# Optimization experiments

Measured on AMD Instinct MI355X. Metric: run time of the kernel, lower is better.

Reference implementation:

```python
import jax, jax.numpy as jnp
import numpy as np

LOW_RANK = 8   # q passed to torch.svd_lowrank
NITER = 2      # torch.svd_lowrank default power-iteration count


def setup_inputs() -> dict:
    key = jax.random.key(0)
    k1, k2 = jax.random.split(key)
    x = jax.random.normal(k1, (32, 256, 56, 56), dtype=jnp.float32)
    # Gaussian test matrix used by torch.svd_lowrank's range finder on A^T:
    # R = randn(A.mT.shape[-1]=C, q), shared across the (H*W) batch.
    omega = jax.random.normal(k2, (256, LOW_RANK), dtype=jnp.float32)
    return {"x": x, "omega": omega}


def _qr_q(a):
    # reduced QR, batched over leading dims; inputs are tall (m >= n)
    return jnp.linalg.qr(a, mode="reduced")[0]


def reference(x, omega):
    B, C, H, W = x.shape
    # [B,C,H,W] -> [H,W,C,B] -> (H*W, C, B): H*W small matrices A of shape (C, B)
    A = jnp.transpose(x, (2, 3, 1, 0)).reshape(H * W, C, B)

    # torch.svd_lowrank with n=B > q takes the transposed branch:
    #   Q = get_approximate_basis(A^T, q, niter=2)   (Q: (B, q), orthonormal cols)
    #   U S V^T == (A @ Q) @ Q^T  -> reconstruction is A Q Q^T
    Y = jnp.einsum("mcb,cq->mbq", A, omega)      # A^T @ Omega : (M, B, q)
    Q = _qr_q(Y)
    for _ in range(NITER):
        Z = jnp.einsum("mcb,mbq->mcq", A, Q)     # A @ Q       : (M, C, q)
        Qc = _qr_q(Z)
        Y = jnp.einsum("mcb,mcq->mbq", A, Qc)    # A^T @ Qc    : (M, B, q)
        Q = _qr_q(Y)

    P = jnp.einsum("mcb,mbq->mcq", A, Q)         # A @ Q       : (M, C, q)
    y = jnp.einsum("mcq,mbq->mcb", P, Q)         # A Q Q^T     : (M, C, B)

    y = y.reshape(H, W, C, B)
    return jnp.transpose(y, (3, 2, 0, 1))        # back to [B, C, H, W]
```

## Files before the change

### kernel.cpp

```cpp
#include <hip/hip_runtime.h>
#include <math.h>

#define HW   3136
#define NB   32
#define NC   256
#define TM   16
#define CC   8
#define LDP  36
#define SLABC (TM * LDP)
#define SLABF (CC * SLABC)

#define NS   4
#define CSL  (NC / NS)
#define NCH  (CSL / CC)
#define GK   1280

#define YT_(mi,b,q) Sm[(mi)*265 + (q)*33 + (b)]
#define WT_(mi,b,q) Sm[4240 + (mi)*265 + (q)*33 + (b)]
#define SS_(mi,k)   Sm[8480 + (mi)*65 + (k)]
#define SMEMF 9520

__host__ __device__ constexpr int TRI(int i, int j) { return i*8 - (i*(i+1))/2 + j; }

__device__ __forceinline__ void stage_load512(float4* r, const float* __restrict__ xg,
                                              int c0, int m0, int t) {
#pragma unroll
  for (int i = 0; i < 2; ++i) {
    int id = t + i * 512;
    int cc = id >> 7, b = (id >> 2) & 31, mq = id & 3;
    r[i] = *reinterpret_cast<const float4*>(
        xg + (size_t)(b * NC + c0 + cc) * HW + m0 + mq * 4);
  }
}
__device__ __forceinline__ void stage_write_t(const float4* r, float* sl, int t) {
#pragma unroll
  for (int i = 0; i < 2; ++i) {
    int id = t + i * 512;
    int cc = id >> 7, b = (id >> 2) & 31, mq = id & 3;
    float* p = sl + cc * SLABC + (mq * 4) * LDP + b;
    p[0 * LDP] = r[i].x;
    p[1 * LDP] = r[i].y;
    p[2 * LDP] = r[i].z;
    p[3 * LDP] = r[i].w;
  }
}

__device__ __forceinline__ void chol8(const float* __restrict__ Sm, int mi, float* Rl) {
#pragma unroll
  for (int i = 0; i < 8; ++i) {
    float d = SS_(mi, i * 8 + i);
#pragma unroll
    for (int k = 0; k < 8; ++k) {
      if (k < i) { float rk = Rl[TRI(k, i)]; d = fmaf(-rk, rk, d); }
    }
    float rii = sqrtf(fmaxf(d, 1e-30f));
    float inv = 1.0f / rii;
    Rl[TRI(i, i)] = inv;
#pragma unroll
    for (int j = 0; j < 8; ++j) {
      if (j > i) {
        float v = SS_(mi, i * 8 + j);
#pragma unroll
        for (int k = 0; k < 8; ++k) {
          if (k < i) v = fmaf(-Rl[TRI(k, i)], Rl[TRI(k, j)], v);
        }
        Rl[TRI(i, j)] = v * inv;
      }
    }
  }
}

__device__ __forceinline__ void trsm1row(const float* __restrict__ srcB, float* __restrict__ dstB,
                                         int mi, int r, const float* Rl) {
  float yv[8], qv[8];
#pragma unroll
  for (int q = 0; q < 8; ++q) yv[q] = srcB[mi * 265 + q * 33 + r];
#pragma unroll
  for (int j = 0; j < 8; ++j) {
    float a = yv[j];
#pragma unroll
    for (int k = 0; k < 8; ++k) {
      if (k < j) a = fmaf(-qv[k], Rl[TRI(k, j)], a);
    }
    qv[j] = a * Rl[TRI(j, j)];
  }
#pragma unroll
  for (int q = 0; q < 8; ++q) dstB[mi * 265 + q * 33 + r] = qv[q];
}

__device__ __forceinline__ void cholqr32(float* __restrict__ Sm, int mi, int r) {
#pragma unroll
  for (int e = 0; e < 2; ++e) {
    int idx = r + e * 32, i = idx >> 3, j = idx & 7;
    float s = 0.f;
#pragma unroll
    for (int b = 0; b < 32; ++b) s = fmaf(YT_(mi, b, i), YT_(mi, b, j), s);
    SS_(mi, idx) = s;
  }
  __syncthreads();
  float Rl[36];
  chol8(Sm, mi, Rl);
  trsm1row(Sm, Sm, mi, r, Rl);
  __syncthreads();
}

__global__ __launch_bounds__(512, 4) void tsvd_k1a(const float* __restrict__ x,
                                                   const float* __restrict__ omega,
                                                   float* __restrict__ Gp) {
  __shared__ float Sm[2 * SLABF];
  const int t = threadIdx.x;
  const int mi = t & 15, r = t >> 4;
  const int s = blockIdx.x & (NS - 1);
  const int mt = blockIdx.x / NS;
  const int m0 = mt * TM, m = m0 + mi;
  const int c0 = s * CSL;

  float G[32], Y[8];
#pragma unroll
  for (int b = 0; b < 32; ++b) G[b] = 0.f;
#pragma unroll
  for (int q = 0; q < 8; ++q) Y[q] = 0.f;

  float4 st[2];
  stage_load512(st, x, c0, m0, t);
  stage_write_t(st, Sm, t);
  for (int ch = 0; ch < NCH; ++ch) {
    if (ch + 1 < NCH) stage_load512(st, x, c0 + (ch + 1) * CC, m0, t);
    __syncthreads();
    const float* cur = Sm + (ch & 1) * SLABF;
#pragma unroll
    for (int cc = 0; cc < CC; ++cc) {
      const int c = c0 + ch * CC + cc;
      const float* v = cur + cc * SLABC + mi * LDP;
      const float ar = v[r];
#pragma unroll
      for (int k = 0; k < 8; ++k) {
        float4 vb = *reinterpret_cast<const float4*>(v + 4 * k);
        G[4 * k + 0] = fmaf(ar, vb.x, G[4 * k + 0]);
        G[4 * k + 1] = fmaf(ar, vb.y, G[4 * k + 1]);
        G[4 * k + 2] = fmaf(ar, vb.z, G[4 * k + 2]);
        G[4 * k + 3] = fmaf(ar, vb.w, G[4 * k + 3]);
      }
#pragma unroll
      for (int q = 0; q < 8; ++q) Y[q] = fmaf(ar, omega[c * 8 + q], Y[q]);
    }
    if (ch + 1 < NCH) stage_write_t(st, Sm + ((ch + 1) & 1) * SLABF, t);
  }

  float4* rec = reinterpret_cast<float4*>(Gp + ((size_t)s * HW + m) * GK);
#pragma unroll
  for (int k = 0; k < 8; ++k)
    rec[r * 8 + k] = make_float4(G[4 * k + 0], G[4 * k + 1], G[4 * k + 2], G[4 * k + 3]);
  rec[256 + r * 2 + 0] = make_float4(Y[0], Y[1], Y[2], Y[3]);
  rec[256 + r * 2 + 1] = make_float4(Y[4], Y[5], Y[6], Y[7]);
}

__global__ __launch_bounds__(256) void tsvd_k1b(const float* __restrict__ Gp,
                                                float* __restrict__ Mws) {
  __shared__ float Sm[SMEMF];
  const int t = threadIdx.x;
  const int r = t & 31, mi = t >> 5;
  const int m0 = blockIdx.x * 8, m = m0 + mi;

  float G0[32], Y0[8];
#pragma unroll
  for (int b = 0; b < 32; ++b) G0[b] = 0.f;
#pragma unroll
  for (int q = 0; q < 8; ++q) Y0[q] = 0.f;
#pragma unroll
  for (int s = 0; s < NS; ++s) {
    const float4* rec = reinterpret_cast<const float4*>(Gp + ((size_t)s * HW + m) * GK);
#pragma unroll
    for (int k = 0; k < 8; ++k) {
      float4 v = rec[r * 8 + k];
      G0[4 * k + 0] += v.x;
      G0[4 * k + 1] += v.y;
      G0[4 * k + 2] += v.z;
      G0[4 * k + 3] += v.w;
    }
    float4 y0 = rec[256 + r * 2 + 0];
    float4 y1 = rec[256 + r * 2 + 1];
    Y0[0] += y0.x; Y0[1] += y0.y; Y0[2] += y0.z; Y0[3] += y0.w;
    Y0[4] += y1.x; Y0[5] += y1.y; Y0[6] += y1.z; Y0[7] += y1.w;
  }

#pragma unroll
  for (int q = 0; q < 8; ++q) YT_(mi, r, q) = Y0[q];
  __syncthreads();

#pragma unroll
  for (int it = 0; it < 3; ++it) {
    cholqr32(Sm, mi, r);
    cholqr32(Sm, mi, r);
    if (it < 2) {
      float u[8];
#pragma unroll
      for (int q = 0; q < 8; ++q) {
        float a = 0.f;
#pragma unroll
        for (int b = 0; b < 32; ++b) a = fmaf(G0[b], YT_(mi, b, q), a);
        u[q] = a;
      }
#pragma unroll
      for (int q = 0; q < 8; ++q) WT_(mi, r, q) = u[q];
      __syncthreads();
#pragma unroll
      for (int e = 0; e < 2; ++e) {
        int idx = r + e * 32, i2 = idx >> 3, j2 = idx & 7;
        float a = 0.f;
#pragma unroll
        for (int b = 0; b < 32; ++b) a = fmaf(YT_(mi, b, i2), WT_(mi, b, j2), a);
        SS_(mi, idx) = a;
      }
      __syncthreads();
      {
        float Rl[36];
        chol8(Sm, mi, Rl);
        trsm1row(Sm, Sm + 4240, mi, r, Rl);
      }
      __syncthreads();
#pragma unroll
      for (int q = 0; q < 8; ++q) {
        float a = 0.f;
#pragma unroll
        for (int b = 0; b < 32; ++b) a = fmaf(G0[b], WT_(mi, b, q), a);
        u[q] = a;
      }
#pragma unroll
      for (int q = 0; q < 8; ++q) YT_(mi, r, q) = u[q];
      __syncthreads();
    }
  }

  float q0[8];
#pragma unroll
  for (int q = 0; q < 8; ++q) q0[q] = YT_(mi, r, q);
  float4* mrec = reinterpret_cast<float4*>(Mws + (size_t)m * 1024);
#pragma unroll
  for (int bq = 0; bq < 8; ++bq) {
    float a[4];
#pragma unroll
    for (int e = 0; e < 4; ++e) {
      int b2 = bq * 4 + e;
      float acc = 0.f;
#pragma unroll
      for (int q = 0; q < 8; ++q) acc = fmaf(q0[q], YT_(mi, b2, q), acc);
      a[e] = acc;
    }
    mrec[r * 8 + bq] = make_float4(a[0], a[1], a[2], a[3]);
  }
}

__global__ __launch_bounds__(512, 4) void tsvd_k2(const float* __restrict__ x,
                                                  const float* __restrict__ Mws,
                                                  float* __restrict__ y) {
  __shared__ float Sm[2 * SLABF];
  const int t = threadIdx.x;
  const int mi = t & 15, r = t >> 4;
  const int bid = blockIdx.x;
  const int mt = bid % 196, cq = bid / 196;
  const int m0 = mt * TM, m = m0 + mi;
  const int cbase = cq * 32;

  float Mc[32];
  {
    const float4* mrec = reinterpret_cast<const float4*>(Mws + (size_t)m * 1024);
#pragma unroll
    for (int k = 0; k < 8; ++k) {
      float4 v = mrec[r * 8 + k];
      Mc[4 * k + 0] = v.x; Mc[4 * k + 1] = v.y; Mc[4 * k + 2] = v.z; Mc[4 * k + 3] = v.w;
    }
  }

  float4 st[2];
  stage_load512(st, x, cbase, m0, t);
  stage_write_t(st, Sm, t);
  for (int ch = 0; ch < 4; ++ch) {
    if (ch + 1 < 4) stage_load512(st, x, cbase + (ch + 1) * CC, m0, t);
    __syncthreads();
    const float* cur = Sm + (ch & 1) * SLABF;
#pragma unroll
    for (int cc = 0; cc < CC; ++cc) {
      const int c = cbase + ch * CC + cc;
      const float* v = cur + cc * SLABC + mi * LDP;
      float a = 0.f;
#pragma unroll
      for (int k = 0; k < 8; ++k) {
        float4 vb = *reinterpret_cast<const float4*>(v + 4 * k);
        a = fmaf(vb.x, Mc[4 * k + 0], a);
        a = fmaf(vb.y, Mc[4 * k + 1], a);
        a = fmaf(vb.z, Mc[4 * k + 2], a);
        a = fmaf(vb.w, Mc[4 * k + 3], a);
      }
      y[((size_t)r * NC + c) * HW + m] = a;
    }
    if (ch + 1 < 4) stage_write_t(st, Sm + ((ch + 1) & 1) * SLABF, t);
  }
}

extern "C" void kernel_launch(void* const* d_in, const int* in_sizes, int n_in,
                              void* d_out, int out_size, void* d_ws, size_t ws_size,
                              hipStream_t stream) {
  const float* x     = (const float*)d_in[0];
  const float* omega = (const float*)d_in[1];
  float* y   = (float*)d_out;
  float* Mws = (float*)d_ws;
  float* Gp  = (float*)d_out;

  tsvd_k1a<<<196 * NS, 512, 0, stream>>>(x, omega, Gp);
  tsvd_k1b<<<HW / 8, 256, 0, stream>>>(Gp, Mws);
  tsvd_k2<<<196 * 8, 512, 0, stream>>>(x, Mws, y);
}
```

Before: 316.3 us.

## Register-tile Gram accumulation and factor projection through rank-8 Q

The Gram kernel now gives each thread an 8x4 register tile of G and a slice of Y. This cuts the shared-memory reads per FMA compared with a full row of 32 per thread. The final kernel stops materialising the 32x32 projector QQ^T per pixel. It stores only Q (32x8) and computes y = (A Q) Q^T in two stages, with P staged in shared memory. That removes the projector build and shrinks workspace traffic, at the cost of an extra barrier and an LDS staging step per chunk.

```diff
diff --git a/kernel.cpp b/kernel.cpp
--- a/kernel.cpp
+++ b/kernel.cpp
@@ -14,6 +14,7 @@
 #define CSL  (NC / NS)
 #define NCH  (CSL / CC)
 #define GK   1280
+#define PST  68
 
 #define YT_(mi,b,q) Sm[(mi)*265 + (q)*33 + (b)]
 #define WT_(mi,b,q) Sm[4240 + (mi)*265 + (q)*33 + (b)]
@@ -109,17 +110,21 @@
                                                    float* __restrict__ Gp) {
   __shared__ float Sm[2 * SLABF];
   const int t = threadIdx.x;
-  const int mi = t & 15, r = t >> 4;
+  const int mi = t & 15, g = t >> 4;
+  const int rg = g >> 3, bj = g & 7;
+  const int r0 = rg * 8, b0 = bj * 4;
   const int s = blockIdx.x & (NS - 1);
   const int mt = blockIdx.x / NS;
   const int m0 = mt * TM, m = m0 + mi;
   const int c0 = s * CSL;
 
-  float G[32], Y[8];
-#pragma unroll
-  for (int b = 0; b < 32; ++b) G[b] = 0.f;
-#pragma unroll
-  for (int q = 0; q < 8; ++q) Y[q] = 0.f;
+  float Gt[8][4], Yt[8];
+#pragma unroll
+  for (int i = 0; i < 8; ++i) {
+    Yt[i] = 0.f;
+#pragma unroll
+    for (int j = 0; j < 4; ++j) Gt[i][j] = 0.f;
+  }
 
   float4 st[2];
   stage_load512(st, x, c0, m0, t);
@@ -132,31 +137,35 @@
     for (int cc = 0; cc < CC; ++cc) {
       const int c = c0 + ch * CC + cc;
       const float* v = cur + cc * SLABC + mi * LDP;
-      const float ar = v[r];
-#pragma unroll
-      for (int k = 0; k < 8; ++k) {
-        float4 vb = *reinterpret_cast<const float4*>(v + 4 * k);
-        G[4 * k + 0] = fmaf(ar, vb.x, G[4 * k + 0]);
-        G[4 * k + 1] = fmaf(ar, vb.y, G[4 * k + 1]);
-        G[4 * k + 2] = fmaf(ar, vb.z, G[4 * k + 2]);
-        G[4 * k + 3] = fmaf(ar, vb.w, G[4 * k + 3]);
-      }
-#pragma unroll
-      for (int q = 0; q < 8; ++q) Y[q] = fmaf(ar, omega[c * 8 + q], Y[q]);
+      float4 ra = *reinterpret_cast<const float4*>(v + r0);
+      float4 rb = *reinterpret_cast<const float4*>(v + r0 + 4);
+      float4 cb = *reinterpret_cast<const float4*>(v + b0);
+      const float w = omega[c * 8 + bj];
+      float rv[8] = {ra.x, ra.y, ra.z, ra.w, rb.x, rb.y, rb.z, rb.w};
+#pragma unroll
+      for (int i = 0; i < 8; ++i) {
+        Gt[i][0] = fmaf(rv[i], cb.x, Gt[i][0]);
+        Gt[i][1] = fmaf(rv[i], cb.y, Gt[i][1]);
+        Gt[i][2] = fmaf(rv[i], cb.z, Gt[i][2]);
+        Gt[i][3] = fmaf(rv[i], cb.w, Gt[i][3]);
+        Yt[i]    = fmaf(rv[i], w,    Yt[i]);
+      }
     }
     if (ch + 1 < NCH) stage_write_t(st, Sm + ((ch + 1) & 1) * SLABF, t);
   }
 
   float4* rec = reinterpret_cast<float4*>(Gp + ((size_t)s * HW + m) * GK);
 #pragma unroll
-  for (int k = 0; k < 8; ++k)
-    rec[r * 8 + k] = make_float4(G[4 * k + 0], G[4 * k + 1], G[4 * k + 2], G[4 * k + 3]);
-  rec[256 + r * 2 + 0] = make_float4(Y[0], Y[1], Y[2], Y[3]);
-  rec[256 + r * 2 + 1] = make_float4(Y[4], Y[5], Y[6], Y[7]);
+  for (int i = 0; i < 8; ++i)
+    rec[(r0 + i) * 8 + bj] = make_float4(Gt[i][0], Gt[i][1], Gt[i][2], Gt[i][3]);
+  float* recf = Gp + ((size_t)s * HW + m) * GK + 1024;
+#pragma unroll
+  for (int i = 0; i < 8; ++i)
+    recf[(r0 + i) * 8 + bj] = Yt[i];
 }
 
 __global__ __launch_bounds__(256) void tsvd_k1b(const float* __restrict__ Gp,
-                                                float* __restrict__ Mws) {
+                                                float* __restrict__ Qws) {
   __shared__ float Sm[SMEMF];
   const int t = threadIdx.x;
   const int r = t & 31, mi = t >> 5;
@@ -235,66 +244,83 @@
   float q0[8];
 #pragma unroll
   for (int q = 0; q < 8; ++q) q0[q] = YT_(mi, r, q);
-  float4* mrec = reinterpret_cast<float4*>(Mws + (size_t)m * 1024);
-#pragma unroll
-  for (int bq = 0; bq < 8; ++bq) {
-    float a[4];
-#pragma unroll
-    for (int e = 0; e < 4; ++e) {
-      int b2 = bq * 4 + e;
-      float acc = 0.f;
-#pragma unroll
-      for (int q = 0; q < 8; ++q) acc = fmaf(q0[q], YT_(mi, b2, q), acc);
-      a[e] = acc;
-    }
-    mrec[r * 8 + bq] = make_float4(a[0], a[1], a[2], a[3]);
-  }
+  float4* qrec = reinterpret_cast<float4*>(Qws + (size_t)m * 256);
+  qrec[r * 2 + 0] = make_float4(q0[0], q0[1], q0[2], q0[3]);
+  qrec[r * 2 + 1] = make_float4(q0[4], q0[5], q0[6], q0[7]);
 }
 
 __global__ __launch_bounds__(512, 4) void tsvd_k2(const float* __restrict__ x,
-                                                  const float* __restrict__ Mws,
+                                                  const float* __restrict__ Qws,
                                                   float* __restrict__ y) {
-  __shared__ float Sm[2 * SLABF];
+  __shared__ float Sm2[2 * SLABF + TM * PST];
+  float* Pl = Sm2 + 2 * SLABF;
   const int t = threadIdx.x;
-  const int mi = t & 15, r = t >> 4;
+  const int mi = t & 15, g = t >> 4;
+  const int cj = g & 7, qd = g >> 3;
+  const int r = g;
   const int bid = blockIdx.x;
   const int mt = bid % 196, cq = bid / 196;
   const int m0 = mt * TM, m = m0 + mi;
   const int cbase = cq * 32;
 
-  float Mc[32];
+  const float* qrec = Qws + (size_t)m * 256;
+  float Qc0[32], Qc1[32];
+#pragma unroll
+  for (int b = 0; b < 32; ++b) {
+    float2 v = reinterpret_cast<const float2*>(qrec)[b * 4 + qd];
+    Qc0[b] = v.x; Qc1[b] = v.y;
+  }
+  float Qr[8];
   {
-    const float4* mrec = reinterpret_cast<const float4*>(Mws + (size_t)m * 1024);
-#pragma unroll
-    for (int k = 0; k < 8; ++k) {
-      float4 v = mrec[r * 8 + k];
-      Mc[4 * k + 0] = v.x; Mc[4 * k + 1] = v.y; Mc[4 * k + 2] = v.z; Mc[4 * k + 3] = v.w;
-    }
+    float4 a = reinterpret_cast<const float4*>(qrec)[r * 2 + 0];
+    float4 b4 = reinterpret_cast<const float4*>(qrec)[r * 2 + 1];
+    Qr[0] = a.x; Qr[1] = a.y; Qr[2] = a.z; Qr[3] = a.w;
+    Qr[4] = b4.x; Qr[5] = b4.y; Qr[6] = b4.z; Qr[7] = b4.w;
   }
 
   float4 st[2];
   stage_load512(st, x, cbase, m0, t);
-  stage_write_t(st, Sm, t);
+  stage_write_t(st, Sm2, t);
   for (int ch = 0; ch < 4; ++ch) {
     if (ch + 1 < 4) stage_load512(st, x, cbase + (ch + 1) * CC, m0, t);
     __syncthreads();
-    const float* cur = Sm + (ch & 1) * SLABF;
-#pragma unroll
-    for (int cc = 0; cc < CC; ++cc) {
-      const int c = cbase + ch * CC + cc;
-      const float* v = cur + cc * SLABC + mi * LDP;
+    const float* cur = Sm2 + (ch & 1) * SLABF;
+    {
+      const float* v = cur + cj * SLABC + mi * LDP;
+      float p0 = 0.f, p1 = 0.f;
+#pragma unroll
+      for (int k = 0; k < 8; ++k) {
+        float4 xb = *reinterpret_cast<const float4*>(v + 4 * k);
+        p0 = fmaf(xb.x, Qc0[4 * k + 0], p0);
+        p0 = fmaf(xb.y, Qc0[4 * k + 1], p0);
+        p0 = fmaf(xb.z, Qc0[4 * k + 2], p0);
+        p0 = fmaf(xb.w, Qc0[4 * k + 3], p0);
+        p1 = fmaf(xb.x, Qc1[4 * k + 0], p1);
+        p1 = fmaf(xb.y, Qc1[4 * k + 1], p1);
+        p1 = fmaf(xb.z, Qc1[4 * k + 2], p1);
+        p1 = fmaf(xb.w, Qc1[4 * k + 3], p1);
+      }
+      *reinterpret_cast<float2*>(Pl + mi * PST + cj * 8 + 2 * qd) = make_float2(p0, p1);
+    }
+    if (ch + 1 < 4) stage_write_t(st, Sm2 + ((ch + 1) & 1) * SLABF, t);
+    __syncthreads();
+    const float* Pm = Pl + mi * PST;
+#pragma unroll
+    for (int c2 = 0; c2 < 8; ++c2) {
+      float4 pa = *reinterpret_cast<const float4*>(Pm + c2 * 8);
+      float4 pb = *reinterpret_cast<const float4*>(Pm + c2 * 8 + 4);
       float a = 0.f;
-#pragma unroll
-      for (int k = 0; k < 8; ++k) {
-        float4 vb = *reinterpret_cast<const float4*>(v + 4 * k);
-        a = fmaf(vb.x, Mc[4 * k + 0], a);
-        a = fmaf(vb.y, Mc[4 * k + 1], a);
-        a = fmaf(vb.z, Mc[4 * k + 2], a);
-        a = fmaf(vb.w, Mc[4 * k + 3], a);
-      }
+      a = fmaf(Qr[0], pa.x, a);
+      a = fmaf(Qr[1], pa.y, a);
+      a = fmaf(Qr[2], pa.z, a);
+      a = fmaf(Qr[3], pa.w, a);
+      a = fmaf(Qr[4], pb.x, a);
+      a = fmaf(Qr[5], pb.y, a);
+      a = fmaf(Qr[6], pb.z, a);
+      a = fmaf(Qr[7], pb.w, a);
+      const int c = cbase + ch * CC + c2;
       y[((size_t)r * NC + c) * HW + m] = a;
     }
-    if (ch + 1 < 4) stage_write_t(st, Sm + ((ch + 1) & 1) * SLABF, t);
   }
 }
 
@@ -304,10 +330,10 @@
   const float* x     = (const float*)d_in[0];
   const float* omega = (const float*)d_in[1];
   float* y   = (float*)d_out;
-  float* Mws = (float*)d_ws;
+  float* Qws = (float*)d_ws;
   float* Gp  = (float*)d_out;
 
   tsvd_k1a<<<196 * NS, 512, 0, stream>>>(x, omega, Gp);
-  tsvd_k1b<<<HW / 8, 256, 0, stream>>>(Gp, Mws);
-  tsvd_k2<<<196 * 8, 512, 0, stream>>>(x, Mws, y);
-}
+  tsvd_k1b<<<HW / 8, 256, 0, stream>>>(Gp, Qws);
+  tsvd_k2<<<196 * 8, 512, 0, stream>>>(x, Qws, y);
+}
```

New measurement: 307.9 us. -2.7%, faster.
